# Kernel optimization log

Measured on AMD Instinct MI355X. Metric: run time of the kernel, lower is better.

Reference implementation:

```python
import jax, jax.numpy as jnp
import numpy as np

D_MODEL = 1024
D_STATE = 16
D_CONV = 4
EXPAND = 2
D_INNER = EXPAND * D_MODEL          # 2048
DT_RANK = D_MODEL // 16             # 64 (ceil(d_model/16))
BATCH = 4
SEQLEN = 2048


def setup_inputs() -> dict:
    key = jax.random.key(0)
    ks = jax.random.split(key, 10)
    s = 0.02
    f32 = jnp.float32
    return {
        "x": jax.random.normal(ks[0], (BATCH, SEQLEN, D_MODEL), f32),
        # RMSNorm
        "rms_w": jnp.ones((D_MODEL,), f32),
        # Mamba params
        "in_w": (jax.random.normal(ks[1], (D_MODEL, 2 * D_INNER), f32) * s),
        "conv_w": (jax.random.normal(ks[2], (D_INNER, D_CONV), f32) * s),
        "conv_b": jnp.zeros((D_INNER,), f32),
        "xproj_w": (jax.random.normal(ks[3], (D_INNER, DT_RANK + 2 * D_STATE), f32) * s),
        "dt_w": (jax.random.normal(ks[4], (DT_RANK, D_INNER), f32) * s),
        "dt_b": jnp.full((D_INNER,), -4.6, f32),  # softplus -> small init dt (mamba-style)
        "A_log": jnp.log(jnp.tile(jnp.arange(1.0, D_STATE + 1.0, dtype=f32), (D_INNER, 1))),
        "Dp": jnp.ones((D_INNER,), f32),
        "out_w": (jax.random.normal(ks[5], (D_INNER, D_MODEL), f32) * s),
        # LayerNorm + GEGLU FFN (mult = expand = 2 -> d_hidden = 2*d_model)
        "ln_w": jnp.ones((D_MODEL,), f32),
        "ln_b": jnp.zeros((D_MODEL,), f32),
        "ff_w1": (jax.random.normal(ks[6], (D_MODEL, 4 * D_MODEL), f32) * s),
        "ff_b1": jnp.zeros((4 * D_MODEL,), f32),
        "ff_w2": (jax.random.normal(ks[7], (2 * D_MODEL, D_MODEL), f32) * s),
        "ff_b2": jnp.zeros((D_MODEL,), f32),
    }


def _mamba(x, in_w, conv_w, conv_b, xproj_w, dt_w, dt_b, A_log, Dp, out_w):
    # x: (B, L, D_MODEL)
    xz = x @ in_w                                   # (B, L, 2*D_INNER)
    xi, z = jnp.split(xz, 2, axis=-1)
    # depthwise causal conv over time
    xc = jnp.transpose(xi, (0, 2, 1))               # (B, D_INNER, L)
    kern = conv_w[:, None, :]                       # (D_INNER, 1, D_CONV)
    xc = jax.lax.conv_general_dilated(
        xc, kern, window_strides=(1,), padding=[(D_CONV - 1, 0)],
        dimension_numbers=("NCH", "OIH", "NCH"), feature_group_count=D_INNER)
    xc = xc + conv_b[None, :, None]
    xi = jax.nn.silu(jnp.transpose(xc, (0, 2, 1)))  # (B, L, D_INNER)
    # input-dependent SSM params
    proj = xi @ xproj_w                             # (B, L, DT_RANK + 2*D_STATE)
    dt, Bm, Cm = jnp.split(proj, [DT_RANK, DT_RANK + D_STATE], axis=-1)
    dt = jax.nn.softplus(dt @ dt_w + dt_b)          # (B, L, D_INNER)
    A = -jnp.exp(A_log)                             # (D_INNER, D_STATE)

    def step(h, inp):
        xt, dtt, Bt, Ct = inp                       # (B,Di), (B,Di), (B,N), (B,N)
        dA = jnp.exp(dtt[:, :, None] * A)           # (B, Di, N)
        h = dA * h + (dtt * xt)[:, :, None] * Bt[:, None, :]
        y = jnp.einsum("bdn,bn->bd", h, Ct)
        return h, y

    h0 = jnp.zeros((xi.shape[0], D_INNER, D_STATE), xi.dtype)
    xs = (jnp.transpose(xi, (1, 0, 2)), jnp.transpose(dt, (1, 0, 2)),
          jnp.transpose(Bm, (1, 0, 2)), jnp.transpose(Cm, (1, 0, 2)))
    _, ys = jax.lax.scan(step, h0, xs)              # ys: (L, B, D_INNER)
    y = jnp.transpose(ys, (1, 0, 2)) + xi * Dp
    y = y * jax.nn.silu(z)
    return y @ out_w                                # (B, L, D_MODEL)


def reference(x, rms_w, in_w, conv_w, conv_b, xproj_w, dt_w, dt_b, A_log, Dp,
              out_w, ln_w, ln_b, ff_w1, ff_b1, ff_w2, ff_b2):
    # RMSNorm + Mamba + residual
    xn = x * jax.lax.rsqrt(jnp.mean(x * x, axis=-1, keepdims=True) + 1e-6) * rms_w
    x = x + _mamba(xn, in_w, conv_w, conv_b, xproj_w, dt_w, dt_b, A_log, Dp, out_w)
    # LayerNorm + GEGLU FFN + residual
    mu = jnp.mean(x, axis=-1, keepdims=True)
    var = jnp.mean((x - mu) ** 2, axis=-1, keepdims=True)
    xn = (x - mu) * jax.lax.rsqrt(var + 1e-5) * ln_w + ln_b
    h = xn @ ff_w1 + ff_b1                          # (B, L, 4*D_MODEL)
    a, g = jnp.split(h, 2, axis=-1)
    ff = (a * jax.nn.gelu(g, approximate=False)) @ ff_w2 + ff_b2
    return x + ff
```

## Files before the change

### kernel.cpp

```cpp
#include <hip/hip_runtime.h>
#include <hip/hip_bf16.h>
#include <cstddef>
#include <cstdint>

#define D_MODEL 1024
#define D_STATE 16
#define D_CONV  4
#define D_INNER 2048
#define DT_RANK 64
#define BATCH   4
#define SEQLEN  2048
#define NTOK    (BATCH * SEQLEN)

#define SCAN_CH 32
#define SCAN_CL 64

typedef unsigned short u16;
typedef __attribute__((ext_vector_type(4))) unsigned short u16x4;
typedef __attribute__((ext_vector_type(8))) short bf16x8;
typedef __attribute__((ext_vector_type(4))) float f32x4;

__device__ __forceinline__ u16 bf16r(float f) {
    union { float f; uint32_t u; } v; v.f = f;
    uint32_t r = v.u + 0x7FFF + ((v.u >> 16) & 1);
    return (u16)(r >> 16);
}
__device__ __forceinline__ float b2f(u16 u) {
    union { uint32_t u; float f; } v; v.u = ((uint32_t)u) << 16;
    return v.f;
}

__device__ __forceinline__ void gload16(const void* g, void* l) {
    __builtin_amdgcn_global_load_lds(
        (const __attribute__((address_space(1))) uint32_t*)g,
        (__attribute__((address_space(3))) uint32_t*)l, 16, 0, 0);
}

__global__ __launch_bounds__(256) void transpose_w_kernel(
    const float* __restrict__ src, int Ksrc, int Nsrc, u16* __restrict__ dst)
{
    __shared__ float t[64][65];
    int k0 = blockIdx.x * 64, n0 = blockIdx.y * 64;
    int tid = threadIdx.x;
    #pragma unroll
    for (int i = 0; i < 16; ++i) {
        int idx = tid + i * 256;
        int r = idx >> 6, c = idx & 63;
        float v = 0.0f;
        if (n0 + c < Nsrc) v = src[(size_t)(k0 + r) * Nsrc + (n0 + c)];
        t[r][c] = v;
    }
    __syncthreads();
    #pragma unroll
    for (int i = 0; i < 16; ++i) {
        int idx = tid + i * 256;
        int r = idx >> 6, c = idx & 63;
        dst[(size_t)(n0 + r) * Ksrc + (k0 + c)] = bf16r(t[c][r]);
    }
}

__global__ __launch_bounds__(256) void rmsnorm_kernel(
    const float* __restrict__ x, const float* __restrict__ w, u16* __restrict__ o)
{
    int row = blockIdx.x;
    const float* xr = x + (size_t)row * D_MODEL;
    float4 v = *reinterpret_cast<const float4*>(xr + threadIdx.x * 4);
    float ss = v.x * v.x + v.y * v.y + v.z * v.z + v.w * v.w;
    #pragma unroll
    for (int off = 32; off > 0; off >>= 1) ss += __shfl_down(ss, off);
    __shared__ float sred[4];
    if ((threadIdx.x & 63) == 0) sred[threadIdx.x >> 6] = ss;
    __syncthreads();
    float tot = sred[0] + sred[1] + sred[2] + sred[3];
    float scale = rsqrtf(tot * (1.0f / D_MODEL) + 1e-6f);
    float4 wv = *reinterpret_cast<const float4*>(w + threadIdx.x * 4);
    u16x4 ov;
    ov[0] = bf16r(v.x * scale * wv.x); ov[1] = bf16r(v.y * scale * wv.y);
    ov[2] = bf16r(v.z * scale * wv.z); ov[3] = bf16r(v.w * scale * wv.w);
    *reinterpret_cast<u16x4*>(o + (size_t)row * D_MODEL + threadIdx.x * 4) = ov;
}

__global__ __launch_bounds__(256) void layernorm_kernel(
    const float* __restrict__ x, const float* __restrict__ w, const float* __restrict__ b,
    u16* __restrict__ o)
{
    int row = blockIdx.x;
    const float* xr = x + (size_t)row * D_MODEL;
    float4 v = *reinterpret_cast<const float4*>(xr + threadIdx.x * 4);
    float s1 = v.x + v.y + v.z + v.w;
    float s2 = v.x * v.x + v.y * v.y + v.z * v.z + v.w * v.w;
    #pragma unroll
    for (int off = 32; off > 0; off >>= 1) {
        s1 += __shfl_down(s1, off);
        s2 += __shfl_down(s2, off);
    }
    __shared__ float r1[4], r2[4];
    if ((threadIdx.x & 63) == 0) { r1[threadIdx.x >> 6] = s1; r2[threadIdx.x >> 6] = s2; }
    __syncthreads();
    float t1 = r1[0] + r1[1] + r1[2] + r1[3];
    float t2 = r2[0] + r2[1] + r2[2] + r2[3];
    float mu = t1 * (1.0f / D_MODEL);
    float var = t2 * (1.0f / D_MODEL) - mu * mu;
    float inv = rsqrtf(var + 1e-5f);
    float4 wv = *reinterpret_cast<const float4*>(w + threadIdx.x * 4);
    float4 bv = *reinterpret_cast<const float4*>(b + threadIdx.x * 4);
    u16x4 ov;
    ov[0] = bf16r((v.x - mu) * inv * wv.x + bv.x);
    ov[1] = bf16r((v.y - mu) * inv * wv.y + bv.y);
    ov[2] = bf16r((v.z - mu) * inv * wv.z + bv.z);
    ov[3] = bf16r((v.w - mu) * inv * wv.w + bv.w);
    *reinterpret_cast<u16x4*>(o + (size_t)row * D_MODEL + threadIdx.x * 4) = ov;
}

template<int EPI>
__global__ __launch_bounds__(256) void gemm_bf16(
    const u16* __restrict__ A, int lda,
    const u16* __restrict__ Bt, int ldb,
    int K, int Nreal,
    float* __restrict__ C, int ldc,
    u16* __restrict__ C2, int ldc2,
    const float* __restrict__ bias,
    const float* __restrict__ res, int ldres)
{
    __shared__ u16 As[2][128 * 32];
    __shared__ u16 Bs[2][128 * 32];
    const int tid = threadIdx.x;
    const int l = tid & 63;
    const int w = tid >> 6;
    const int wm = w >> 1, wn = w & 1;

    int gx = gridDim.x;
    int nwg = gx * gridDim.y;
    int orig = blockIdx.y * gx + blockIdx.x;
    int swz = (orig & 7) * (nwg >> 3) + (orig >> 3);
    const int bm = (swz / gx) * 128, bn = (swz % gx) * 128;
    const int kBeg = blockIdx.z * K;

    f32x4 acc[4][4] = {};

    const char* Ab = (const char*)A + (size_t)bm * lda * 2;
    const char* Bb = (const char*)Bt + (size_t)bn * ldb * 2;
    const int o0 = tid * 16;
    const int row0 = o0 >> 6, col0 = o0 & 63;
    const int nIter = K >> 5;

    auto stage = [&](int buf, int j) {
        const int kb = (kBeg + j * 32) * 2;
        u16* AsW = As[buf] + (w << 9);
        u16* BsW = Bs[buf] + (w << 9);
        gload16(Ab + (size_t)row0 * (lda * 2) + kb + col0, AsW);
        gload16(Ab + (size_t)(row0 + 64) * (lda * 2) + kb + col0, AsW + 2048);
        gload16(Bb + (size_t)row0 * (ldb * 2) + kb + col0, BsW);
        gload16(Bb + (size_t)(row0 + 64) * (ldb * 2) + kb + col0, BsW + 2048);
    };

    stage(0, 0);
    __syncthreads();

    const int half16 = (l >> 4) << 4;
    for (int j = 0; j < nIter; ++j) {
        const int buf = j & 1;
        if (j + 1 < nIter) stage(buf ^ 1, j + 1);
        bf16x8 af[4], bfr[4];
        #pragma unroll
        for (int m = 0; m < 4; ++m) {
            int r = wm * 64 + m * 16 + (l & 15);
            af[m] = *reinterpret_cast<const bf16x8*>((const char*)As[buf] + r * 64 + half16);
        }
        #pragma unroll
        for (int n = 0; n < 4; ++n) {
            int r = wn * 64 + n * 16 + (l & 15);
            bfr[n] = *reinterpret_cast<const bf16x8*>((const char*)Bs[buf] + r * 64 + half16);
        }
        #pragma unroll
        for (int m = 0; m < 4; ++m)
            #pragma unroll
            for (int n = 0; n < 4; ++n)
                acc[m][n] = __builtin_amdgcn_mfma_f32_16x16x32_bf16(
                    af[m], bfr[n], acc[m][n], 0, 0, 0);
        __syncthreads();
    }

    const int cr0 = (l >> 4) * 4;
    const int cc = l & 15;
    #pragma unroll
    for (int m = 0; m < 4; ++m) {
        #pragma unroll
        for (int n = 0; n < 4; ++n) {
            #pragma unroll
            for (int r = 0; r < 4; ++r) {
                int row = bm + wm * 64 + m * 16 + cr0 + r;
                int col = bn + wn * 64 + n * 16 + cc;
                if (col >= Nreal) continue;
                float t = acc[m][n][r];
                if (EPI == 3 || EPI == 5 || EPI == 6) t += bias[col];
                if (EPI == 3) t = (t > 20.0f) ? t : __logf(1.0f + __expf(t));
                if (EPI == 4 || EPI == 6) t += res[(size_t)row * ldres + col];
                if (EPI == 0 || EPI == 3 || EPI == 4 || EPI == 6)
                    C[(size_t)row * ldc + col] = t;
                if (EPI == 1 || EPI == 5)
                    C2[(size_t)row * ldc2 + col] = bf16r(t);
                if (EPI == 7)
                    atomicAdd(&C[(size_t)row * ldc + col], t);
            }
        }
    }
}

__global__ __launch_bounds__(256) void cast_bf16_kernel(
    const float* __restrict__ src, u16* __restrict__ dst, int n4)
{
    int idx = blockIdx.x * 256 + threadIdx.x;
    if (idx >= n4) return;
    float4 v = *reinterpret_cast<const float4*>(src + idx * 4);
    u16x4 o;
    o[0] = bf16r(v.x); o[1] = bf16r(v.y); o[2] = bf16r(v.z); o[3] = bf16r(v.w);
    *reinterpret_cast<u16x4*>(dst + idx * 4) = o;
}

__global__ __launch_bounds__(256) void conv_silu_kernel(
    const u16* __restrict__ xr, const float* __restrict__ cw,
    const float* __restrict__ cb, u16* __restrict__ xi)
{
    int idx = blockIdx.x * 256 + threadIdx.x;
    if (idx >= NTOK * D_INNER) return;
    int d = idx & (D_INNER - 1);
    int bt = idx >> 11;
    int t = bt & (SEQLEN - 1);
    const u16* base = xr + (size_t)bt * D_INNER + d;
    float w0 = cw[d * 4 + 0], w1 = cw[d * 4 + 1], w2 = cw[d * 4 + 2], w3 = cw[d * 4 + 3];
    float acc = cb[d] + w3 * b2f(base[0]);
    if (t >= 1) acc += w2 * b2f(base[-(ptrdiff_t)D_INNER]);
    if (t >= 2) acc += w1 * b2f(base[-(ptrdiff_t)(2 * D_INNER)]);
    if (t >= 3) acc += w0 * b2f(base[-(ptrdiff_t)(3 * D_INNER)]);
    float s = acc / (1.0f + __expf(-acc));
    xi[idx] = bf16r(s);
}

__global__ __launch_bounds__(256) void scan_phaseA(
    const u16* __restrict__ xi,
    const float* __restrict__ dtv,
    const float* __restrict__ proj,
    const float* __restrict__ A_log,
    float* __restrict__ sum)
{
    int c  = blockIdx.x & (SCAN_CH - 1);
    int dg = (blockIdx.x >> 5) & 7;
    int b  = blockIdx.x >> 8;
    int d  = (dg << 8) + threadIdx.x;
    float A[D_STATE], h[D_STATE], P[D_STATE];
    #pragma unroll
    for (int n = 0; n < D_STATE; ++n) {
        A[n] = -__expf(A_log[(size_t)d * D_STATE + n]);
        h[n] = 0.0f;
        P[n] = 1.0f;
    }
    __shared__ float sBC[32][33];
    const float* prow = proj + ((size_t)b * SEQLEN + (size_t)c * SCAN_CL) * 96;
    for (int sub = 0; sub < SCAN_CL / 32; ++sub) {
        __syncthreads();
        {
            int s = threadIdx.x >> 3;
            int k4 = (threadIdx.x & 7) * 4;
            float4 v = *reinterpret_cast<const float4*>(
                prow + (size_t)(sub * 32 + s) * 96 + 64 + k4);
            sBC[s][k4 + 0] = v.x; sBC[s][k4 + 1] = v.y;
            sBC[s][k4 + 2] = v.z; sBC[s][k4 + 3] = v.w;
        }
        __syncthreads();
        for (int s2 = 0; s2 < 32; ++s2) {
            int t = c * SCAN_CL + sub * 32 + s2;
            size_t base = ((size_t)b * SEQLEN + t) * D_INNER + d;
            float xt = b2f(xi[base]);
            float dtt = dtv[base];
            float dbx = dtt * xt;
            #pragma unroll
            for (int n = 0; n < D_STATE; ++n) {
                float dA = __expf(dtt * A[n]);
                h[n] = dA * h[n] + dbx * sBC[s2][n];
                P[n] *= dA;
            }
        }
    }
    size_t sbase = (((size_t)b * SCAN_CH + c) * 32) * D_INNER + d;
    #pragma unroll
    for (int n = 0; n < D_STATE; ++n) {
        sum[sbase + (size_t)n * D_INNER] = P[n];
        sum[sbase + (size_t)(16 + n) * D_INNER] = h[n];
    }
}

__global__ __launch_bounds__(256) void scan_phaseB(float* __restrict__ sum)
{
    int idx = blockIdx.x * 256 + threadIdx.x;
    int b = idx >> 11;
    int d = idx & (D_INNER - 1);
    float h[D_STATE];
    #pragma unroll
    for (int n = 0; n < D_STATE; ++n) h[n] = 0.0f;
    for (int c = 0; c < SCAN_CH; ++c) {
        size_t sb = (((size_t)b * SCAN_CH + c) * 32) * D_INNER + d;
        #pragma unroll
        for (int n = 0; n < D_STATE; ++n) {
            float P  = sum[sb + (size_t)n * D_INNER];
            float Hl = sum[sb + (size_t)(16 + n) * D_INNER];
            sum[sb + (size_t)(16 + n) * D_INNER] = h[n];
            h[n] = P * h[n] + Hl;
        }
    }
}

__global__ __launch_bounds__(256) void scan_phaseC(
    const u16* __restrict__ xi,
    const float* __restrict__ dtv,
    const float* __restrict__ proj,
    const float* __restrict__ A_log,
    const float* __restrict__ Dp,
    const u16* __restrict__ z,
    const float* __restrict__ sum,
    u16* __restrict__ yb)
{
    int c  = blockIdx.x & (SCAN_CH - 1);
    int dg = (blockIdx.x >> 5) & 7;
    int b  = blockIdx.x >> 8;
    int d  = (dg << 8) + threadIdx.x;
    float A[D_STATE], h[D_STATE];
    size_t sbase = (((size_t)b * SCAN_CH + c) * 32) * D_INNER + d;
    #pragma unroll
    for (int n = 0; n < D_STATE; ++n) {
        A[n] = -__expf(A_log[(size_t)d * D_STATE + n]);
        h[n] = sum[sbase + (size_t)(16 + n) * D_INNER];
    }
    float dp = Dp[d];
    __shared__ float sBC[32][33];
    const float* prow = proj + ((size_t)b * SEQLEN + (size_t)c * SCAN_CL) * 96;
    for (int sub = 0; sub < SCAN_CL / 32; ++sub) {
        __syncthreads();
        {
            int s = threadIdx.x >> 3;
            int k4 = (threadIdx.x & 7) * 4;
            float4 v = *reinterpret_cast<const float4*>(
                prow + (size_t)(sub * 32 + s) * 96 + 64 + k4);
            sBC[s][k4 + 0] = v.x; sBC[s][k4 + 1] = v.y;
            sBC[s][k4 + 2] = v.z; sBC[s][k4 + 3] = v.w;
        }
        __syncthreads();
        for (int s2 = 0; s2 < 32; ++s2) {
            int t = c * SCAN_CL + sub * 32 + s2;
            size_t base = ((size_t)b * SEQLEN + t) * D_INNER + d;
            float xt = b2f(xi[base]);
            float dtt = dtv[base];
            float dbx = dtt * xt;
            float yv = 0.0f;
            #pragma unroll
            for (int n = 0; n < D_STATE; ++n) {
                float dA = __expf(dtt * A[n]);
                h[n] = dA * h[n] + dbx * sBC[s2][n];
                yv += h[n] * sBC[s2][D_STATE + n];
            }
            float zv = b2f(z[base]);
            float sz = zv / (1.0f + __expf(-zv));
            yb[base] = bf16r((yv + xt * dp) * sz);
        }
    }
}

__global__ __launch_bounds__(256) void gelu_gate_kernel(
    const u16* __restrict__ hff, u16* __restrict__ o)
{
    int idx = blockIdx.x * 256 + threadIdx.x;
    if (idx >= NTOK * D_INNER / 4) return;
    int e = idx * 4;
    int j = e & (D_INNER - 1);
    int bt = e >> 11;
    const u16* hrow = hff + (size_t)bt * (2 * D_INNER);
    u16x4 av = *reinterpret_cast<const u16x4*>(hrow + j);
    u16x4 gv = *reinterpret_cast<const u16x4*>(hrow + D_INNER + j);
    u16x4 ov;
    #pragma unroll
    for (int k = 0; k < 4; ++k) {
        float fa = b2f(av[k]), fg = b2f(gv[k]);
        ov[k] = bf16r(fa * fg * 0.5f * (1.0f + erff(fg * 0.70710678118f)));
    }
    *reinterpret_cast<u16x4*>(o + (size_t)bt * D_INNER + j) = ov;
}

extern "C" void kernel_launch(void* const* d_in, const int* in_sizes, int n_in,
                              void* d_out, int out_size, void* d_ws, size_t ws_size,
                              hipStream_t stream)
{
    const float* x       = (const float*)d_in[0];
    const float* rms_w   = (const float*)d_in[1];
    const float* in_w    = (const float*)d_in[2];
    const float* conv_w  = (const float*)d_in[3];
    const float* conv_b  = (const float*)d_in[4];
    const float* xproj_w = (const float*)d_in[5];
    const float* dt_w    = (const float*)d_in[6];
    const float* dt_b    = (const float*)d_in[7];
    const float* A_log   = (const float*)d_in[8];
    const float* Dp      = (const float*)d_in[9];
    const float* out_w   = (const float*)d_in[10];
    const float* ln_w    = (const float*)d_in[11];
    const float* ln_b    = (const float*)d_in[12];
    const float* ff_w1   = (const float*)d_in[13];
    const float* ff_b1   = (const float*)d_in[14];
    const float* ff_w2   = (const float*)d_in[15];
    const float* ff_b2   = (const float*)d_in[16];
    float* out = (float*)d_out;

    char* p = (char*)d_ws;
    float* P0f  = (float*)p;
    u16*   hff  = (u16*)p;        p += (size_t)NTOK * D_INNER * 4;
    u16*   zb   = (u16*)p;
    u16*   agb  = zb;             p += (size_t)NTOK * D_INNER * 2;
    u16*   xirb = (u16*)p;
    u16*   ybf  = xirb;           p += (size_t)NTOK * D_INNER * 2;
    u16*   xnb  = (u16*)p;        p += (size_t)NTOK * D_MODEL * 2;
    float* proj = (float*)p;      p += (size_t)NTOK * 96 * 4;
    float* sum  = (float*)p;      p += (size_t)BATCH * SCAN_CH * 32 * D_INNER * 4;
    u16*   xib  = (u16*)p;        p += (size_t)NTOK * D_INNER * 2;
    u16*   projb= (u16*)p;        p += (size_t)NTOK * 96 * 2;
    u16*   inwT = (u16*)p;        p += (size_t)4096 * 1024 * 2;
    u16*   xpT  = (u16*)p;        p += (size_t)128 * 2048 * 2;
    u16*   dtwT = (u16*)p;        p += (size_t)2048 * 64 * 2;
    u16*   owT  = (u16*)p;        p += (size_t)1024 * 2048 * 2;
    u16*   f1T  = (u16*)p;        p += (size_t)4096 * 1024 * 2;
    u16*   f2T  = (u16*)p;        p += (size_t)1024 * 2048 * 2;

    hipLaunchKernelGGL(transpose_w_kernel, dim3(16, 64), dim3(256), 0, stream, in_w,    1024, 4096, inwT);
    hipLaunchKernelGGL(transpose_w_kernel, dim3(32, 2),  dim3(256), 0, stream, xproj_w, 2048,   96, xpT);
    hipLaunchKernelGGL(transpose_w_kernel, dim3(1, 32),  dim3(256), 0, stream, dt_w,      64, 2048, dtwT);
    hipLaunchKernelGGL(transpose_w_kernel, dim3(32, 16), dim3(256), 0, stream, out_w,   2048, 1024, owT);
    hipLaunchKernelGGL(transpose_w_kernel, dim3(16, 64), dim3(256), 0, stream, ff_w1,   1024, 4096, f1T);
    hipLaunchKernelGGL(transpose_w_kernel, dim3(32, 16), dim3(256), 0, stream, ff_w2,   2048, 1024, f2T);

    hipLaunchKernelGGL(rmsnorm_kernel, dim3(NTOK), dim3(256), 0, stream, x, rms_w, xnb);
    hipLaunchKernelGGL((gemm_bf16<1>), dim3(16, 64), dim3(256), 0, stream,
                       xnb, D_MODEL, inwT, D_MODEL, D_MODEL, D_INNER,
                       (float*)nullptr, 0, xirb, D_INNER, nullptr, nullptr, 0);
    hipLaunchKernelGGL((gemm_bf16<1>), dim3(16, 64), dim3(256), 0, stream,
                       xnb, D_MODEL, inwT + (size_t)D_INNER * D_MODEL, D_MODEL, D_MODEL, D_INNER,
                       (float*)nullptr, 0, zb, D_INNER, nullptr, nullptr, 0);
    hipLaunchKernelGGL(conv_silu_kernel, dim3((NTOK * D_INNER + 255) / 256), dim3(256), 0, stream,
                       xirb, conv_w, conv_b, xib);
    hipMemsetAsync(proj, 0, (size_t)NTOK * 96 * 4, stream);
    hipLaunchKernelGGL((gemm_bf16<7>), dim3(1, 64, 8), dim3(256), 0, stream,
                       xib, D_INNER, xpT, D_INNER, D_INNER / 8, 96,
                       proj, 96, (u16*)nullptr, 0, nullptr, nullptr, 0);
    hipLaunchKernelGGL(cast_bf16_kernel, dim3(NTOK * 96 / 4 / 256), dim3(256), 0, stream,
                       proj, projb, NTOK * 96 / 4);
    hipLaunchKernelGGL((gemm_bf16<3>), dim3(16, 64), dim3(256), 0, stream,
                       projb, 96, dtwT, DT_RANK, DT_RANK, D_INNER,
                       P0f, D_INNER, (u16*)nullptr, 0, dt_b, nullptr, 0);
    hipLaunchKernelGGL(scan_phaseA, dim3(BATCH * 8 * SCAN_CH), dim3(256), 0, stream,
                       xib, P0f, proj, A_log, sum);
    hipLaunchKernelGGL(scan_phaseB, dim3(32), dim3(256), 0, stream, sum);
    hipLaunchKernelGGL(scan_phaseC, dim3(BATCH * 8 * SCAN_CH), dim3(256), 0, stream,
                       xib, P0f, proj, A_log, Dp, zb, sum, ybf);
    hipLaunchKernelGGL((gemm_bf16<4>), dim3(8, 64), dim3(256), 0, stream,
                       ybf, D_INNER, owT, D_INNER, D_INNER, D_MODEL,
                       out, D_MODEL, (u16*)nullptr, 0, nullptr, x, D_MODEL);
    hipLaunchKernelGGL(layernorm_kernel, dim3(NTOK), dim3(256), 0, stream, out, ln_w, ln_b, xnb);
    hipLaunchKernelGGL((gemm_bf16<5>), dim3(32, 64), dim3(256), 0, stream,
                       xnb, D_MODEL, f1T, D_MODEL, D_MODEL, 4 * D_MODEL,
                       (float*)nullptr, 0, hff, 4 * D_MODEL, ff_b1, nullptr, 0);
    hipLaunchKernelGGL(gelu_gate_kernel, dim3((NTOK * D_INNER / 4 + 255) / 256), dim3(256), 0, stream,
                       hff, agb);
    hipLaunchKernelGGL((gemm_bf16<6>), dim3(8, 64), dim3(256), 0, stream,
                       agb, D_INNER, f2T, D_INNER, D_INNER, D_MODEL,
                       out, D_MODEL, (u16*)nullptr, 0, ff_b2, out, D_MODEL);
}
```

Measured before the change: 812.9 us.

## Fuse GEGLU into FF1 GEMM epilogue via interleaved weights; split scan states across thread pairs

Transposes ff_w1 so the value and gate columns sit in adjacent interleaved positions. The FF1 GEMM epilogue then computes a*gelu(g) by pairing lanes with a shuffle and writes the bf16 gated activation directly. This removes the separate gelu_gate kernel and the round trip through the 4*D_MODEL intermediate. The selective scan phases A and C now split the 16 states across two threads per channel, with a shuffle reduction for y. That doubles the thread count to raise parallelism and lower per-thread register use, at the cost of redundant loads of x, dt and z.

```diff
diff --git a/kernel.cpp b/kernel.cpp
--- a/kernel.cpp
+++ b/kernel.cpp
@@ -56,6 +56,30 @@
         int idx = tid + i * 256;
         int r = idx >> 6, c = idx & 63;
         dst[(size_t)(n0 + r) * Ksrc + (k0 + c)] = bf16r(t[c][r]);
+    }
+}
+
+__global__ __launch_bounds__(256) void transpose_w1_kernel(
+    const float* __restrict__ src, u16* __restrict__ dst)
+{
+    const int Ksrc = 1024, Nsrc = 4096;
+    __shared__ float t[64][65];
+    int k0 = blockIdx.x * 64, n0 = blockIdx.y * 64;
+    int tid = threadIdx.x;
+    #pragma unroll
+    for (int i = 0; i < 16; ++i) {
+        int idx = tid + i * 256;
+        int r = idx >> 6, c = idx & 63;
+        t[r][c] = src[(size_t)(k0 + r) * Nsrc + (n0 + c)];
+    }
+    __syncthreads();
+    #pragma unroll
+    for (int i = 0; i < 16; ++i) {
+        int idx = tid + i * 256;
+        int r = idx >> 6, c = idx & 63;
+        int j = n0 + r;
+        int pj = (j < 2048) ? (2 * j) : (2 * (j - 2048) + 1);
+        dst[(size_t)pj * Ksrc + (k0 + c)] = bf16r(t[c][r]);
     }
 }
 
@@ -191,6 +215,16 @@
             for (int r = 0; r < 4; ++r) {
                 int row = bm + wm * 64 + m * 16 + cr0 + r;
                 int col = bn + wn * 64 + n * 16 + cc;
+                if (EPI == 8) {
+                    int origc = (col >> 1) + (col & 1) * 2048;
+                    float t = acc[m][n][r] + bias[origc];
+                    float tg = __shfl_xor(t, 1);
+                    if ((l & 1) == 0) {
+                        float val = t * tg * 0.5f * (1.0f + erff(tg * 0.70710678118f));
+                        C2[(size_t)row * ldc2 + (col >> 1)] = bf16r(val);
+                    }
+                    continue;
+                }
                 if (col >= Nreal) continue;
                 float t = acc[m][n][r];
                 if (EPI == 3 || EPI == 5 || EPI == 6) t += bias[col];
@@ -244,16 +278,18 @@
     const float* __restrict__ A_log,
     float* __restrict__ sum)
 {
-    int c  = blockIdx.x & (SCAN_CH - 1);
-    int dg = (blockIdx.x >> 5) & 7;
-    int b  = blockIdx.x >> 8;
-    int d  = (dg << 8) + threadIdx.x;
-    float A[D_STATE], h[D_STATE], P[D_STATE];
-    #pragma unroll
-    for (int n = 0; n < D_STATE; ++n) {
-        A[n] = -__expf(A_log[(size_t)d * D_STATE + n]);
-        h[n] = 0.0f;
-        P[n] = 1.0f;
+    int c    = blockIdx.x & (SCAN_CH - 1);
+    int dg   = (blockIdx.x >> 5) & 15;
+    int b    = blockIdx.x >> 9;
+    int half = threadIdx.x & 1;
+    int d    = (dg << 7) + (threadIdx.x >> 1);
+    const int n0 = half * 8;
+    float A[8], h[8], P[8];
+    #pragma unroll
+    for (int j = 0; j < 8; ++j) {
+        A[j] = -__expf(A_log[(size_t)d * D_STATE + n0 + j]);
+        h[j] = 0.0f;
+        P[j] = 1.0f;
     }
     __shared__ float sBC[32][33];
     const float* prow = proj + ((size_t)b * SEQLEN + (size_t)c * SCAN_CL) * 96;
@@ -275,18 +311,18 @@
             float dtt = dtv[base];
             float dbx = dtt * xt;
             #pragma unroll
-            for (int n = 0; n < D_STATE; ++n) {
-                float dA = __expf(dtt * A[n]);
-                h[n] = dA * h[n] + dbx * sBC[s2][n];
-                P[n] *= dA;
+            for (int j = 0; j < 8; ++j) {
+                float dA = __expf(dtt * A[j]);
+                h[j] = dA * h[j] + dbx * sBC[s2][n0 + j];
+                P[j] *= dA;
             }
         }
     }
     size_t sbase = (((size_t)b * SCAN_CH + c) * 32) * D_INNER + d;
     #pragma unroll
-    for (int n = 0; n < D_STATE; ++n) {
-        sum[sbase + (size_t)n * D_INNER] = P[n];
-        sum[sbase + (size_t)(16 + n) * D_INNER] = h[n];
+    for (int j = 0; j < 8; ++j) {
+        sum[sbase + (size_t)(n0 + j) * D_INNER] = P[j];
+        sum[sbase + (size_t)(16 + n0 + j) * D_INNER] = h[j];
     }
 }
 
@@ -320,16 +356,18 @@
     const float* __restrict__ sum,
     u16* __restrict__ yb)
 {
-    int c  = blockIdx.x & (SCAN_CH - 1);
-    int dg = (blockIdx.x >> 5) & 7;
-    int b  = blockIdx.x >> 8;
-    int d  = (dg << 8) + threadIdx.x;
-    float A[D_STATE], h[D_STATE];
+    int c    = blockIdx.x & (SCAN_CH - 1);
+    int dg   = (blockIdx.x >> 5) & 15;
+    int b    = blockIdx.x >> 9;
+    int half = threadIdx.x & 1;
+    int d    = (dg << 7) + (threadIdx.x >> 1);
+    const int n0 = half * 8;
+    float A[8], h[8];
     size_t sbase = (((size_t)b * SCAN_CH + c) * 32) * D_INNER + d;
     #pragma unroll
-    for (int n = 0; n < D_STATE; ++n) {
-        A[n] = -__expf(A_log[(size_t)d * D_STATE + n]);
-        h[n] = sum[sbase + (size_t)(16 + n) * D_INNER];
+    for (int j = 0; j < 8; ++j) {
+        A[j] = -__expf(A_log[(size_t)d * D_STATE + n0 + j]);
+        h[j] = sum[sbase + (size_t)(16 + n0 + j) * D_INNER];
     }
     float dp = Dp[d];
     __shared__ float sBC[32][33];
@@ -353,36 +391,19 @@
             float dbx = dtt * xt;
             float yv = 0.0f;
             #pragma unroll
-            for (int n = 0; n < D_STATE; ++n) {
-                float dA = __expf(dtt * A[n]);
-                h[n] = dA * h[n] + dbx * sBC[s2][n];
-                yv += h[n] * sBC[s2][D_STATE + n];
+            for (int j = 0; j < 8; ++j) {
+                float dA = __expf(dtt * A[j]);
+                h[j] = dA * h[j] + dbx * sBC[s2][n0 + j];
+                yv += h[j] * sBC[s2][16 + n0 + j];
             }
-            float zv = b2f(z[base]);
-            float sz = zv / (1.0f + __expf(-zv));
-            yb[base] = bf16r((yv + xt * dp) * sz);
-        }
-    }
-}
-
-__global__ __launch_bounds__(256) void gelu_gate_kernel(
-    const u16* __restrict__ hff, u16* __restrict__ o)
-{
-    int idx = blockIdx.x * 256 + threadIdx.x;
-    if (idx >= NTOK * D_INNER / 4) return;
-    int e = idx * 4;
-    int j = e & (D_INNER - 1);
-    int bt = e >> 11;
-    const u16* hrow = hff + (size_t)bt * (2 * D_INNER);
-    u16x4 av = *reinterpret_cast<const u16x4*>(hrow + j);
-    u16x4 gv = *reinterpret_cast<const u16x4*>(hrow + D_INNER + j);
-    u16x4 ov;
-    #pragma unroll
-    for (int k = 0; k < 4; ++k) {
-        float fa = b2f(av[k]), fg = b2f(gv[k]);
-        ov[k] = bf16r(fa * fg * 0.5f * (1.0f + erff(fg * 0.70710678118f)));
-    }
-    *reinterpret_cast<u16x4*>(o + (size_t)bt * D_INNER + j) = ov;
+            yv += __shfl_xor(yv, 1);
+            if (half == 0) {
+                float zv = b2f(z[base]);
+                float sz = zv / (1.0f + __expf(-zv));
+                yb[base] = bf16r((yv + xt * dp) * sz);
+            }
+        }
+    }
 }
 
 extern "C" void kernel_launch(void* const* d_in, const int* in_sizes, int n_in,
@@ -409,8 +430,7 @@
     float* out = (float*)d_out;
 
     char* p = (char*)d_ws;
-    float* P0f  = (float*)p;
-    u16*   hff  = (u16*)p;        p += (size_t)NTOK * D_INNER * 4;
+    float* P0f  = (float*)p;      p += (size_t)NTOK * D_INNER * 4;
     u16*   zb   = (u16*)p;
     u16*   agb  = zb;             p += (size_t)NTOK * D_INNER * 2;
     u16*   xirb = (u16*)p;
@@ -431,7 +451,7 @@
     hipLaunchKernelGGL(transpose_w_kernel, dim3(32, 2),  dim3(256), 0, stream, xproj_w, 2048,   96, xpT);
     hipLaunchKernelGGL(transpose_w_kernel, dim3(1, 32),  dim3(256), 0, stream, dt_w,      64, 2048, dtwT);
     hipLaunchKernelGGL(transpose_w_kernel, dim3(32, 16), dim3(256), 0, stream, out_w,   2048, 1024, owT);
-    hipLaunchKernelGGL(transpose_w_kernel, dim3(16, 64), dim3(256), 0, stream, ff_w1,   1024, 4096, f1T);
+    hipLaunchKernelGGL(transpose_w1_kernel, dim3(16, 64), dim3(256), 0, stream, ff_w1, f1T);
     hipLaunchKernelGGL(transpose_w_kernel, dim3(32, 16), dim3(256), 0, stream, ff_w2,   2048, 1024, f2T);
 
     hipLaunchKernelGGL(rmsnorm_kernel, dim3(NTOK), dim3(256), 0, stream, x, rms_w, xnb);
@@ -452,20 +472,18 @@
     hipLaunchKernelGGL((gemm_bf16<3>), dim3(16, 64), dim3(256), 0, stream,
                        projb, 96, dtwT, DT_RANK, DT_RANK, D_INNER,
                        P0f, D_INNER, (u16*)nullptr, 0, dt_b, nullptr, 0);
-    hipLaunchKernelGGL(scan_phaseA, dim3(BATCH * 8 * SCAN_CH), dim3(256), 0, stream,
+    hipLaunchKernelGGL(scan_phaseA, dim3(BATCH * 16 * SCAN_CH), dim3(256), 0, stream,
                        xib, P0f, proj, A_log, sum);
     hipLaunchKernelGGL(scan_phaseB, dim3(32), dim3(256), 0, stream, sum);
-    hipLaunchKernelGGL(scan_phaseC, dim3(BATCH * 8 * SCAN_CH), dim3(256), 0, stream,
+    hipLaunchKernelGGL(scan_phaseC, dim3(BATCH * 16 * SCAN_CH), dim3(256), 0, stream,
                        xib, P0f, proj, A_log, Dp, zb, sum, ybf);
     hipLaunchKernelGGL((gemm_bf16<4>), dim3(8, 64), dim3(256), 0, stream,
                        ybf, D_INNER, owT, D_INNER, D_INNER, D_MODEL,
                        out, D_MODEL, (u16*)nullptr, 0, nullptr, x, D_MODEL);
     hipLaunchKernelGGL(layernorm_kernel, dim3(NTOK), dim3(256), 0, stream, out, ln_w, ln_b, xnb);
-    hipLaunchKernelGGL((gemm_bf16<5>), dim3(32, 64), dim3(256), 0, stream,
+    hipLaunchKernelGGL((gemm_bf16<8>), dim3(32, 64), dim3(256), 0, stream,
                        xnb, D_MODEL, f1T, D_MODEL, D_MODEL, 4 * D_MODEL,
-                       (float*)nullptr, 0, hff, 4 * D_MODEL, ff_b1, nullptr, 0);
-    hipLaunchKernelGGL(gelu_gate_kernel, dim3((NTOK * D_INNER / 4 + 255) / 256), dim3(256), 0, stream,
-                       hff, agb);
+                       (float*)nullptr, 0, agb, D_INNER, ff_b1, nullptr, 0);
     hipLaunchKernelGGL((gemm_bf16<6>), dim3(8, 64), dim3(256), 0, stream,
                        agb, D_INNER, f2T, D_INNER, D_INNER, D_MODEL,
                        out, D_MODEL, (u16*)nullptr, 0, ff_b2, out, D_MODEL);
```

After: 835.4 us. +2.8%, slower.
